# Performance work log

Hardware: AMD Instinct MI355X
Metric: run time of the kernel (lower is better)

Reference implementation:

```python
import jax, jax.numpy as jnp
import numpy as np
import math

N, L, E_IN, MDL, H, NE = 8, 4096, 512, 512, 8, 131072
D = MDL // H


def setup_inputs() -> dict:
    key = jax.random.key(0)
    ks = jax.random.split(key, 12)
    s_in = 1.0 / math.sqrt(E_IN)
    s_md = 1.0 / math.sqrt(MDL)
    return {
        "queries": jax.random.normal(ks[0], (N, L, E_IN), jnp.float32),
        "keys": jax.random.normal(ks[1], (N, L, E_IN), jnp.float32),
        "values": jax.random.normal(ks[2], (N, L, E_IN), jnp.float32),
        "adj": jax.random.randint(ks[3], (2, NE), 0, L, jnp.int32),
        "Wq": jax.random.normal(ks[4], (MDL, E_IN), jnp.float32) * s_in,
        "bq": jnp.zeros((MDL,), jnp.float32),
        "Wk": jax.random.normal(ks[5], (MDL, E_IN), jnp.float32) * s_in,
        "bk": jnp.zeros((MDL,), jnp.float32),
        "Wv": jax.random.normal(ks[6], (MDL, E_IN), jnp.float32) * s_in,
        "bv": jnp.zeros((MDL,), jnp.float32),
        "Wfc": jax.random.normal(ks[7], (MDL, MDL), jnp.float32) * s_md,
        "bfc": jnp.zeros((MDL,), jnp.float32),
    }


def _split_head(x):
    n, l, c = x.shape
    return jnp.transpose(x.reshape(n, l, H, c // H), (0, 2, 1, 3))  # (n,h,l,d)


def reference(queries, keys, values, adj, Wq, bq, Wk, bk, Wv, bv, Wfc, bfc):
    q = _split_head(queries @ Wq.T + bq)  # (n,h,l,e)
    k = _split_head(keys @ Wk.T + bk)
    v = _split_head(values @ Wv.T + bv)
    n, h, l, e = q.shape
    temp = 1.0 / math.sqrt(e)
    row, col = adj[0], adj[1]  # query idx / key idx per edge
    # edge-wise QK dot products: (n,h,E)
    qk = temp * jnp.einsum('nhed,nhed->nhe', q[:, :, row, :], k[:, :, col, :])
    # segment softmax over edges grouped by query node (adj[0])
    qk_t = jnp.transpose(qk, (2, 0, 1))  # (E,n,h) - segment ops act on axis 0
    m = jax.ops.segment_max(qk_t, row, num_segments=l)  # (L,n,h)
    ex = jnp.exp(qk_t - m[row])
    den = jax.ops.segment_sum(ex, row, num_segments=l)
    a = ex / den[row]  # (E,n,h); dropout is identity in eval mode
    # spmm: out[i] += a[edge] * v[j] for each edge (i=row, j=col)
    vj = jnp.transpose(v[:, :, col, :], (2, 0, 1, 3))  # (E,n,h,d)
    agg = jax.ops.segment_sum(vj * a[..., None], row, num_segments=l)  # (L,n,h,d)
    out = jnp.transpose(agg, (1, 0, 2, 3)).reshape(n, l, h * e)  # (n,l,h*d)
    return out @ Wfc.T + bfc
```

## Files before the change

### kernel.cpp

```cpp
#include <hip/hip_runtime.h>
#include <cstdint>

typedef __attribute__((ext_vector_type(8))) short short8;
typedef __attribute__((ext_vector_type(8))) _Float16 half8;
typedef __attribute__((ext_vector_type(2))) _Float16 h2;
typedef __attribute__((ext_vector_type(2))) __fp16 fp16x2;
typedef __attribute__((ext_vector_type(4))) float f32x4;

#define AS1 __attribute__((address_space(1)))
#define AS3 __attribute__((address_space(3)))

constexpr int NB   = 8;
constexpr int L    = 4096;
constexpr int CH   = 512;
constexpr int DD   = 64;
constexpr int NE   = 131072;
constexpr int M_ROWS = NB * L;

template <int CTRL>
__device__ __forceinline__ float dppadd(float s) {
    union { float f; int i; } u, r;
    u.f = s;
    r.i = __builtin_amdgcn_update_dpp(0, u.i, CTRL, 0xF, 0xF, true);
    return s + r.f;
}

__global__ __launch_bounds__(256)
void cvt8_k(const float* __restrict__ src, _Float16* __restrict__ dst) {
    const int i = blockIdx.x * 256 + threadIdx.x;
    const f32x4 a = ((const f32x4*)src)[i * 2];
    const f32x4 b = ((const f32x4*)src)[i * 2 + 1];
    fp16x2 h[4];
    h[0] = __builtin_amdgcn_cvt_pkrtz(a.x, a.y);
    h[1] = __builtin_amdgcn_cvt_pkrtz(a.z, a.w);
    h[2] = __builtin_amdgcn_cvt_pkrtz(b.x, b.y);
    h[3] = __builtin_amdgcn_cvt_pkrtz(b.z, b.w);
    half8 out;
    __builtin_memcpy(&out, h, 16);
    ((half8*)dst)[i] = out;
}

__global__ __launch_bounds__(256)
void cvtw_k(const float* __restrict__ s0, const float* __restrict__ s1,
            const float* __restrict__ s2, const float* __restrict__ s3,
            _Float16* __restrict__ dst) {
    const float* s = (blockIdx.y == 0) ? s0 : (blockIdx.y == 1) ? s1
                   : (blockIdx.y == 2) ? s2 : s3;
    _Float16* d = dst + (size_t)blockIdx.y * (CH * CH);
    const int i = blockIdx.x * 256 + threadIdx.x;
    const f32x4 a = ((const f32x4*)s)[i * 2];
    const f32x4 b = ((const f32x4*)s)[i * 2 + 1];
    fp16x2 h[4];
    h[0] = __builtin_amdgcn_cvt_pkrtz(a.x, a.y);
    h[1] = __builtin_amdgcn_cvt_pkrtz(a.z, a.w);
    h[2] = __builtin_amdgcn_cvt_pkrtz(b.x, b.y);
    h[3] = __builtin_amdgcn_cvt_pkrtz(b.z, b.w);
    half8 out;
    __builtin_memcpy(&out, h, 16);
    ((half8*)d)[i] = out;
}

template <bool OUT_F32>
__global__ __launch_bounds__(256)
void gemm_f16(const _Float16* __restrict__ A, const _Float16* __restrict__ B,
              const float* __restrict__ bias, void* __restrict__ Cp)
{
    __shared__ _Float16 As[128 * 64];
    __shared__ _Float16 Bs[128 * 64];
    const int bid = blockIdx.x;
    const int swz = (bid & 7) * 128 + (bid >> 3);
    const int row0 = (swz >> 2) * 128;
    const int col0 = (swz & 3) * 128;
    const int t = threadIdx.x, lane = t & 63, wid = t >> 6;
    const int wm = (wid >> 1) * 64, wn = (wid & 1) * 64;
    const int fr = lane & 15, fkb = (lane >> 4) * 8;
    const int srow = lane >> 3;
    const int scol = (lane & 7) * 8;

    f32x4 acc[4][4] = {};

    for (int k0 = 0; k0 < CH; k0 += 64) {
#pragma unroll
        for (int q = 0; q < 4; q++) {
            const int r = wid * 32 + q * 8;
            __builtin_amdgcn_global_load_lds(
                (const AS1 unsigned int*)
                    (A + (size_t)(row0 + r + srow) * CH + k0 + scol),
                (AS3 unsigned int*)(As + r * 64), 16, 0, 0);
        }
#pragma unroll
        for (int q = 0; q < 4; q++) {
            const int r = wid * 32 + q * 8;
            __builtin_amdgcn_global_load_lds(
                (const AS1 unsigned int*)
                    (B + (size_t)(col0 + r + srow) * CH + k0 + scol),
                (AS3 unsigned int*)(Bs + r * 64), 16, 0, 0);
        }
        __syncthreads();
#pragma unroll
        for (int kk = 0; kk < 2; kk++) {
            half8 afr[4], bfr[4];
#pragma unroll
            for (int f = 0; f < 4; f++)
                afr[f] = *(const half8*)&As[(wm + f * 16 + fr) * 64 + kk * 32 + fkb];
#pragma unroll
            for (int f = 0; f < 4; f++)
                bfr[f] = *(const half8*)&Bs[(wn + f * 16 + fr) * 64 + kk * 32 + fkb];
#pragma unroll
            for (int fm = 0; fm < 4; fm++)
#pragma unroll
                for (int fn = 0; fn < 4; fn++)
                    acc[fm][fn] = __builtin_amdgcn_mfma_f32_16x16x32_f16(
                        afr[fm], bfr[fn], acc[fm][fn], 0, 0, 0);
        }
        __syncthreads();
    }

    const int rsub = (lane >> 4) * 4;
#pragma unroll
    for (int fn = 0; fn < 4; fn++) {
        const int gc = col0 + wn + fn * 16 + fr;
        const float bv = bias[gc];
#pragma unroll
        for (int fm = 0; fm < 4; fm++) {
            const int gr = row0 + wm + fm * 16 + rsub;
#pragma unroll
            for (int j = 0; j < 4; j++) {
                const float v = acc[fm][fn][j] + bv;
                if constexpr (OUT_F32)
                    ((float*)Cp)[(size_t)(gr + j) * CH + gc] = v;
                else
                    ((_Float16*)Cp)[(size_t)(gr + j) * CH + gc] = (_Float16)v;
            }
        }
    }
}

__global__ void zero_k(int* cnt, int* fill) {
    int i = blockIdx.x * blockDim.x + threadIdx.x;
    if (i < L) { cnt[i] = 0; fill[i] = 0; }
}
__global__ void count_k(const int* __restrict__ adj, int* __restrict__ cnt) {
    int e = blockIdx.x * blockDim.x + threadIdx.x;
    if (e < NE) atomicAdd(&cnt[adj[e]], 1);
}
__global__ void scan_k(const int* __restrict__ cnt, int* __restrict__ rowptr) {
    const int lane = threadIdx.x;
    const int base = lane * 64;
    int s = 0;
    for (int t2 = 0; t2 < 64; t2++) s += cnt[base + t2];
    int incl = s;
    for (int off = 1; off < 64; off <<= 1) {
        int v = __shfl_up(incl, off);
        if (lane >= off) incl += v;
    }
    int run = incl - s;
    for (int t2 = 0; t2 < 64; t2++) { rowptr[base + t2] = run; run += cnt[base + t2]; }
    if (lane == 63) rowptr[L] = run;
}
__global__ void scatter_k(const int* __restrict__ adj, const int* __restrict__ rowptr,
                          int* __restrict__ fill, int* __restrict__ ecol) {
    int e = blockIdx.x * blockDim.x + threadIdx.x;
    if (e < NE) {
        int rr = adj[e];
        int pos = rowptr[rr] + atomicAdd(&fill[rr], 1);
        ecol[pos] = adj[NE + e];
    }
}

__global__ __launch_bounds__(256)
void attn_k(const _Float16* __restrict__ qb, const _Float16* __restrict__ kb,
            const _Float16* __restrict__ vb, const int* __restrict__ rowptr,
            const int* __restrict__ ecol, _Float16* __restrict__ agg)
{
    __shared__ float part[4 * 8 * 65];
    const int bid = blockIdx.x;
    const int n   = bid & 7;
    const int rem = bid >> 3;
    const int hg  = rem >> 12;
    const int i   = rem & 4095;
    const int lane = threadIdx.x & 63;
    const int w    = threadIdx.x >> 6;
    const int h    = hg * 4 + w;
    const int g    = lane & 7;
    const int grp  = lane >> 3;
    const size_t rowbase = ((size_t)(n * L + i)) * CH + h * DD;

    fp16x2 qq[4];
    {
        const half8 qu = *(const half8*)(qb + rowbase + g * 8);
        const _Float16 sc = (_Float16)(0.125f * 1.44269504088896f);
        h2 qh[4];
#pragma unroll
        for (int e = 0; e < 4; e++) {
            qh[e][0] = qu[2 * e] * sc;
            qh[e][1] = qu[2 * e + 1] * sc;
        }
        __builtin_memcpy(qq, qh, 16);
    }
    const int start = rowptr[i], end = rowptr[i + 1];
    const char* kb_u = (const char*)(kb + (size_t)n * L * CH + h * DD);
    const char* vb_u = (const char*)(vb + (size_t)n * L * CH + h * DD);
    const int goff = g << 4;

    h2 oA[4] = {}, oB[4] = {};
    float lsA = 0.f, lsB = 0.f;

    const int nIt = (end - start + 15) >> 4;
    int idx = start + grp;
    const int last = end - 1;
    half8 kA{}, vA{}, kB{}, vB{};
    int jA1 = 0, jB1 = 0;
    if (nIt > 0) {
        const int jA0 = ecol[min(idx, last)];
        const int jB0 = ecol[min(idx + 8, last)];
        kA = *(const half8*)(kb_u + ((jA0 << 10) + goff));
        vA = *(const half8*)(vb_u + ((jA0 << 10) + goff));
        kB = *(const half8*)(kb_u + ((jB0 << 10) + goff));
        vB = *(const half8*)(vb_u + ((jB0 << 10) + goff));
        jA1 = ecol[min(idx + 16, last)];
        jB1 = ecol[min(idx + 24, last)];
    }

    for (int it = 0; it < nIt; ++it) {
        const half8 kAn = *(const half8*)(kb_u + ((jA1 << 10) + goff));
        const half8 vAn = *(const half8*)(vb_u + ((jA1 << 10) + goff));
        const half8 kBn = *(const half8*)(kb_u + ((jB1 << 10) + goff));
        const half8 vBn = *(const half8*)(vb_u + ((jB1 << 10) + goff));
        const int jA2 = ecol[min(idx + 32, last)];
        const int jB2 = ecol[min(idx + 40, last)];
        const bool vdA = idx < end;
        const bool vdB = idx + 8 < end;
        fp16x2 ka[4], kb2[4];
        __builtin_memcpy(ka, &kA, 16);
        __builtin_memcpy(kb2, &kB, 16);
        float sA = 0.f, sB = 0.f;
#if __has_builtin(__builtin_amdgcn_fdot2)
#pragma unroll
        for (int e = 0; e < 4; e++) {
            sA = __builtin_amdgcn_fdot2(ka[e],  qq[e], sA, false);
            sB = __builtin_amdgcn_fdot2(kb2[e], qq[e], sB, false);
        }
#else
#pragma unroll
        for (int e = 0; e < 4; e++) {
            sA = fmaf((float)ka[e][0],  (float)qq[e][0], sA);
            sA = fmaf((float)ka[e][1],  (float)qq[e][1], sA);
            sB = fmaf((float)kb2[e][0], (float)qq[e][0], sB);
            sB = fmaf((float)kb2[e][1], (float)qq[e][1], sB);
        }
#endif
        sA = dppadd<0xB1>(sA);  sB = dppadd<0xB1>(sB);
        sA = dppadd<0x4E>(sA);  sB = dppadd<0x4E>(sB);
        sA = dppadd<0x141>(sA); sB = dppadd<0x141>(sB);
        float peA = exp2f(sA); peA = vdA ? peA : 0.f;
        float peB = exp2f(sB); peB = vdB ? peB : 0.f;
        const _Float16 phA = (_Float16)peA, phB = (_Float16)peB;
        const h2 pa2 = {phA, phA}, pb2 = {phB, phB};
        h2 va2[4], vb2[4];
        __builtin_memcpy(va2, &vA, 16);
        __builtin_memcpy(vb2, &vB, 16);
#pragma unroll
        for (int e = 0; e < 4; e++) {
            oA[e] += pa2 * va2[e];
            oB[e] += pb2 * vb2[e];
        }
        lsA += peA; lsB += peB;
        kA = kAn; vA = vAn; kB = kBn; vB = vBn;
        jA1 = jA2; jB1 = jB2; idx += 16;
    }

    float lsum = lsA + lsB;
    lsum += __shfl_xor(lsum, 8);
    lsum += __shfl_xor(lsum, 16);
    lsum += __shfl_xor(lsum, 32);

    float o[8];
#pragma unroll
    for (int e = 0; e < 4; e++) {
        o[2 * e]     = (float)oA[e][0] + (float)oB[e][0];
        o[2 * e + 1] = (float)oA[e][1] + (float)oB[e][1];
    }
    float* p = part + w * (8 * 65);
    float* pw = p + grp * 65 + g * 8;
    *(f32x4*)(pw)     = *(f32x4*)&o[0];
    *(f32x4*)(pw + 4) = *(f32x4*)&o[4];
    __builtin_amdgcn_s_waitcnt(0);
    float osum = 0.f;
#pragma unroll
    for (int gg = 0; gg < 8; gg++)
        osum += p[gg * 65 + lane];

    const float inv = (end > start) ? 1.f / lsum : 0.f;
    agg[rowbase + lane] = (_Float16)(osum * inv);
}

extern "C" void kernel_launch(void* const* d_in, const int* in_sizes, int n_in,
                              void* d_out, int out_size, void* d_ws, size_t ws_size,
                              hipStream_t stream)
{
    (void)in_sizes; (void)n_in; (void)out_size; (void)ws_size;
    const float* queries = (const float*)d_in[0];
    const float* keys    = (const float*)d_in[1];
    const float* values  = (const float*)d_in[2];
    const int*   adj     = (const int*)d_in[3];
    const float* Wq  = (const float*)d_in[4];
    const float* bq  = (const float*)d_in[5];
    const float* Wk  = (const float*)d_in[6];
    const float* bk  = (const float*)d_in[7];
    const float* Wv  = (const float*)d_in[8];
    const float* bv  = (const float*)d_in[9];
    const float* Wfc = (const float*)d_in[10];
    const float* bfc = (const float*)d_in[11];

    _Float16* qb = (_Float16*)d_out;
    _Float16* kb = qb + (size_t)M_ROWS * CH;
    uint8_t* w = (uint8_t*)d_ws;
    _Float16* vb  = (_Float16*)(w);
    _Float16* agg = (_Float16*)(w + 33554432);
    _Float16* wf  = (_Float16*)(w + 67108864);
    int* cnt    = (int*)(w + 69206016);
    int* fill   = (int*)(w + 69206016 + 16384);
    int* rowptr = (int*)(w + 69206016 + 32768);
    int* ecol   = (int*)(w + 69206016 + 65536);

    _Float16* stg = agg;
    constexpr int WELEM = CH * CH;

    cvtw_k<<<dim3(WELEM / (256 * 8), 4), 256, 0, stream>>>(Wq, Wk, Wv, Wfc, wf);

    zero_k<<<(L + 255) / 256, 256, 0, stream>>>(cnt, fill);
    count_k<<<(NE + 255) / 256, 256, 0, stream>>>(adj, cnt);
    scan_k<<<1, 64, 0, stream>>>(cnt, rowptr);
    scatter_k<<<(NE + 255) / 256, 256, 0, stream>>>(adj, rowptr, fill, ecol);

    dim3 gg(1024);
    cvt8_k<<<M_ROWS * CH / (256 * 8), 256, 0, stream>>>(queries, stg);
    gemm_f16<false><<<gg, 256, 0, stream>>>(stg, wf + 0 * WELEM, bq, qb);
    cvt8_k<<<M_ROWS * CH / (256 * 8), 256, 0, stream>>>(keys, stg);
    gemm_f16<false><<<gg, 256, 0, stream>>>(stg, wf + 1 * WELEM, bk, kb);
    cvt8_k<<<M_ROWS * CH / (256 * 8), 256, 0, stream>>>(values, stg);
    gemm_f16<false><<<gg, 256, 0, stream>>>(stg, wf + 2 * WELEM, bv, vb);

    attn_k<<<dim3(2 * NB * L), 256, 0, stream>>>(qb, kb, vb, rowptr, ecol, agg);

    gemm_f16<true><<<gg, 256, 0, stream>>>(agg, wf + 3 * WELEM, bfc, (float*)d_out);
}
```

Before: 344.8 us.

## Fuse independent prep stages into horizontally merged kernels with double staging

Merges the weight conversion, CSR construction steps and input conversions into four horizontally fused launches. Each GEMM for Q/K/V shares its grid with the fp16 conversion of the next input, using a second staging buffer. This cuts the number of launches and lets memory-bound conversion blocks overlap with MFMA GEMM blocks. The fused path only runs if the workspace is large enough; otherwise the old sequence is kept. Fused kernels reserve GEMM shared memory even for conversion blocks, which may limit their occupancy.

```diff
diff --git a/kernel.cpp b/kernel.cpp
--- a/kernel.cpp
+++ b/kernel.cpp
@@ -16,6 +16,7 @@
 constexpr int DD   = 64;
 constexpr int NE   = 131072;
 constexpr int M_ROWS = NB * L;
+constexpr int WELEM  = CH * CH;
 
 template <int CTRL>
 __device__ __forceinline__ float dppadd(float s) {
@@ -25,9 +26,10 @@
     return s + r.f;
 }
 
-__global__ __launch_bounds__(256)
-void cvt8_k(const float* __restrict__ src, _Float16* __restrict__ dst) {
-    const int i = blockIdx.x * 256 + threadIdx.x;
+
+__device__ __forceinline__ void cvt_body(int bid, const float* __restrict__ src,
+                                         _Float16* __restrict__ dst) {
+    const int i = bid * 256 + (int)threadIdx.x;
     const f32x4 a = ((const f32x4*)src)[i * 2];
     const f32x4 b = ((const f32x4*)src)[i * 2 + 1];
     fp16x2 h[4];
@@ -40,14 +42,88 @@
     ((half8*)dst)[i] = out;
 }
 
-__global__ __launch_bounds__(256)
-void cvtw_k(const float* __restrict__ s0, const float* __restrict__ s1,
-            const float* __restrict__ s2, const float* __restrict__ s3,
-            _Float16* __restrict__ dst) {
-    const float* s = (blockIdx.y == 0) ? s0 : (blockIdx.y == 1) ? s1
-                   : (blockIdx.y == 2) ? s2 : s3;
-    _Float16* d = dst + (size_t)blockIdx.y * (CH * CH);
-    const int i = blockIdx.x * 256 + threadIdx.x;
+template <bool OUT_F32>
+__device__ __forceinline__ void gemm_body(int bid, _Float16* As, _Float16* Bs,
+                                          const _Float16* __restrict__ A,
+                                          const _Float16* __restrict__ B,
+                                          const float* __restrict__ bias,
+                                          void* __restrict__ Cp)
+{
+    const int swz = (bid & 7) * 128 + (bid >> 3);
+    const int row0 = (swz >> 2) * 128;
+    const int col0 = (swz & 3) * 128;
+    const int t = threadIdx.x, lane = t & 63, wid = t >> 6;
+    const int wm = (wid >> 1) * 64, wn = (wid & 1) * 64;
+    const int fr = lane & 15, fkb = (lane >> 4) * 8;
+    const int srow = lane >> 3;
+    const int scol = (lane & 7) * 8;
+
+    f32x4 acc[4][4] = {};
+
+    for (int k0 = 0; k0 < CH; k0 += 64) {
+#pragma unroll
+        for (int q = 0; q < 4; q++) {
+            const int r = wid * 32 + q * 8;
+            __builtin_amdgcn_global_load_lds(
+                (const AS1 unsigned int*)
+                    (A + (size_t)(row0 + r + srow) * CH + k0 + scol),
+                (AS3 unsigned int*)(As + r * 64), 16, 0, 0);
+        }
+#pragma unroll
+        for (int q = 0; q < 4; q++) {
+            const int r = wid * 32 + q * 8;
+            __builtin_amdgcn_global_load_lds(
+                (const AS1 unsigned int*)
+                    (B + (size_t)(col0 + r + srow) * CH + k0 + scol),
+                (AS3 unsigned int*)(Bs + r * 64), 16, 0, 0);
+        }
+        __syncthreads();
+#pragma unroll
+        for (int kk = 0; kk < 2; kk++) {
+            half8 afr[4], bfr[4];
+#pragma unroll
+            for (int f = 0; f < 4; f++)
+                afr[f] = *(const half8*)&As[(wm + f * 16 + fr) * 64 + kk * 32 + fkb];
+#pragma unroll
+            for (int f = 0; f < 4; f++)
+                bfr[f] = *(const half8*)&Bs[(wn + f * 16 + fr) * 64 + kk * 32 + fkb];
+#pragma unroll
+            for (int fm = 0; fm < 4; fm++)
+#pragma unroll
+                for (int fn = 0; fn < 4; fn++)
+                    acc[fm][fn] = __builtin_amdgcn_mfma_f32_16x16x32_f16(
+                        afr[fm], bfr[fn], acc[fm][fn], 0, 0, 0);
+        }
+        __syncthreads();
+    }
+
+    const int rsub = (lane >> 4) * 4;
+#pragma unroll
+    for (int fn = 0; fn < 4; fn++) {
+        const int gc = col0 + wn + fn * 16 + fr;
+        const float bv = bias[gc];
+#pragma unroll
+        for (int fm = 0; fm < 4; fm++) {
+            const int gr = row0 + wm + fm * 16 + rsub;
+#pragma unroll
+            for (int j = 0; j < 4; j++) {
+                const float v = acc[fm][fn][j] + bv;
+                if constexpr (OUT_F32)
+                    ((float*)Cp)[(size_t)(gr + j) * CH + gc] = v;
+                else
+                    ((_Float16*)Cp)[(size_t)(gr + j) * CH + gc] = (_Float16)v;
+            }
+        }
+    }
+}
+
+__device__ __forceinline__ void cvtw_body(int bid, const float* s0, const float* s1,
+                                          const float* s2, const float* s3,
+                                          _Float16* dst) {
+    const int idx = bid * 256 + (int)threadIdx.x;
+    const int wsel = idx >> 15;
+    const float* s = (wsel == 0) ? s0 : (wsel == 1) ? s1 : (wsel == 2) ? s2 : s3;
+    const int i = idx & 32767;
     const f32x4 a = ((const f32x4*)s)[i * 2];
     const f32x4 b = ((const f32x4*)s)[i * 2 + 1];
     fp16x2 h[4];
@@ -57,95 +133,20 @@
     h[3] = __builtin_amdgcn_cvt_pkrtz(b.z, b.w);
     half8 out;
     __builtin_memcpy(&out, h, 16);
-    ((half8*)d)[i] = out;
-}
-
-template <bool OUT_F32>
-__global__ __launch_bounds__(256)
-void gemm_f16(const _Float16* __restrict__ A, const _Float16* __restrict__ B,
-              const float* __restrict__ bias, void* __restrict__ Cp)
-{
-    __shared__ _Float16 As[128 * 64];
-    __shared__ _Float16 Bs[128 * 64];
-    const int bid = blockIdx.x;
-    const int swz = (bid & 7) * 128 + (bid >> 3);
-    const int row0 = (swz >> 2) * 128;
-    const int col0 = (swz & 3) * 128;
-    const int t = threadIdx.x, lane = t & 63, wid = t >> 6;
-    const int wm = (wid >> 1) * 64, wn = (wid & 1) * 64;
-    const int fr = lane & 15, fkb = (lane >> 4) * 8;
-    const int srow = lane >> 3;
-    const int scol = (lane & 7) * 8;
-
-    f32x4 acc[4][4] = {};
-
-    for (int k0 = 0; k0 < CH; k0 += 64) {
-#pragma unroll
-        for (int q = 0; q < 4; q++) {
-            const int r = wid * 32 + q * 8;
-            __builtin_amdgcn_global_load_lds(
-                (const AS1 unsigned int*)
-                    (A + (size_t)(row0 + r + srow) * CH + k0 + scol),
-                (AS3 unsigned int*)(As + r * 64), 16, 0, 0);
-        }
-#pragma unroll
-        for (int q = 0; q < 4; q++) {
-            const int r = wid * 32 + q * 8;
-            __builtin_amdgcn_global_load_lds(
-                (const AS1 unsigned int*)
-                    (B + (size_t)(col0 + r + srow) * CH + k0 + scol),
-                (AS3 unsigned int*)(Bs + r * 64), 16, 0, 0);
-        }
-        __syncthreads();
-#pragma unroll
-        for (int kk = 0; kk < 2; kk++) {
-            half8 afr[4], bfr[4];
-#pragma unroll
-            for (int f = 0; f < 4; f++)
-                afr[f] = *(const half8*)&As[(wm + f * 16 + fr) * 64 + kk * 32 + fkb];
-#pragma unroll
-            for (int f = 0; f < 4; f++)
-                bfr[f] = *(const half8*)&Bs[(wn + f * 16 + fr) * 64 + kk * 32 + fkb];
-#pragma unroll
-            for (int fm = 0; fm < 4; fm++)
-#pragma unroll
-                for (int fn = 0; fn < 4; fn++)
-                    acc[fm][fn] = __builtin_amdgcn_mfma_f32_16x16x32_f16(
-                        afr[fm], bfr[fn], acc[fm][fn], 0, 0, 0);
-        }
-        __syncthreads();
-    }
-
-    const int rsub = (lane >> 4) * 4;
-#pragma unroll
-    for (int fn = 0; fn < 4; fn++) {
-        const int gc = col0 + wn + fn * 16 + fr;
-        const float bv = bias[gc];
-#pragma unroll
-        for (int fm = 0; fm < 4; fm++) {
-            const int gr = row0 + wm + fm * 16 + rsub;
-#pragma unroll
-            for (int j = 0; j < 4; j++) {
-                const float v = acc[fm][fn][j] + bv;
-                if constexpr (OUT_F32)
-                    ((float*)Cp)[(size_t)(gr + j) * CH + gc] = v;
-                else
-                    ((_Float16*)Cp)[(size_t)(gr + j) * CH + gc] = (_Float16)v;
-            }
-        }
-    }
-}
-
-__global__ void zero_k(int* cnt, int* fill) {
-    int i = blockIdx.x * blockDim.x + threadIdx.x;
+    ((half8*)(dst + (size_t)wsel * WELEM))[i] = out;
+}
+
+__device__ __forceinline__ void zero_body(int bid, int* cnt, int* fill) {
+    const int i = bid * 256 + (int)threadIdx.x;
     if (i < L) { cnt[i] = 0; fill[i] = 0; }
 }
-__global__ void count_k(const int* __restrict__ adj, int* __restrict__ cnt) {
-    int e = blockIdx.x * blockDim.x + threadIdx.x;
+__device__ __forceinline__ void count_body(int bid, const int* adj, int* cnt) {
+    const int e = bid * 256 + (int)threadIdx.x;
     if (e < NE) atomicAdd(&cnt[adj[e]], 1);
 }
-__global__ void scan_k(const int* __restrict__ cnt, int* __restrict__ rowptr) {
+__device__ __forceinline__ void scan_body(const int* cnt, int* rowptr) {
     const int lane = threadIdx.x;
+    if (lane >= 64) return;
     const int base = lane * 64;
     int s = 0;
     for (int t2 = 0; t2 < 64; t2++) s += cnt[base + t2];
@@ -158,14 +159,95 @@
     for (int t2 = 0; t2 < 64; t2++) { rowptr[base + t2] = run; run += cnt[base + t2]; }
     if (lane == 63) rowptr[L] = run;
 }
-__global__ void scatter_k(const int* __restrict__ adj, const int* __restrict__ rowptr,
-                          int* __restrict__ fill, int* __restrict__ ecol) {
-    int e = blockIdx.x * blockDim.x + threadIdx.x;
+__device__ __forceinline__ void scatter_body(int bid, const int* adj, const int* rowptr,
+                                             int* fill, int* ecol) {
+    const int e = bid * 256 + (int)threadIdx.x;
     if (e < NE) {
         int rr = adj[e];
         int pos = rowptr[rr] + atomicAdd(&fill[rr], 1);
         ecol[pos] = adj[NE + e];
     }
+}
+
+__global__ __launch_bounds__(256)
+void fusedD0(const float* __restrict__ queries, _Float16* __restrict__ stgA,
+             const float* Wq, const float* Wk, const float* Wv, const float* Wfc,
+             _Float16* __restrict__ wf, int* cnt, int* fill)
+{
+    const int bid = blockIdx.x;
+    if (bid < 8192)       cvt_body(bid, queries, stgA);
+    else if (bid < 8704)  cvtw_body(bid - 8192, Wq, Wk, Wv, Wfc, wf);
+    else                  zero_body(bid - 8704, cnt, fill);
+}
+
+__global__ __launch_bounds__(256)
+void fusedD1(const _Float16* __restrict__ stgA, const _Float16* __restrict__ wf,
+             const float* __restrict__ bq, _Float16* __restrict__ qb,
+             const float* __restrict__ keys, _Float16* __restrict__ stgB,
+             const int* __restrict__ adj, int* cnt)
+{
+    __shared__ _Float16 As[128 * 64];
+    __shared__ _Float16 Bs[128 * 64];
+    const int bid = blockIdx.x;
+    if (bid < 1024)       gemm_body<false>(bid, As, Bs, stgA, wf, bq, qb);
+    else if (bid < 9216)  cvt_body(bid - 1024, keys, stgB);
+    else                  count_body(bid - 9216, adj, cnt);
+}
+
+__global__ __launch_bounds__(256)
+void fusedD2(const _Float16* __restrict__ stgB, const _Float16* __restrict__ wf,
+             const float* __restrict__ bk, _Float16* __restrict__ kb,
+             const float* __restrict__ values, _Float16* __restrict__ stgA,
+             const int* __restrict__ cnt, int* rowptr)
+{
+    __shared__ _Float16 As[128 * 64];
+    __shared__ _Float16 Bs[128 * 64];
+    const int bid = blockIdx.x;
+    if (bid < 1024)       gemm_body<false>(bid, As, Bs, stgB, wf, bk, kb);
+    else if (bid < 9216)  cvt_body(bid - 1024, values, stgA);
+    else                  scan_body(cnt, rowptr);
+}
+
+__global__ __launch_bounds__(256)
+void fusedD3(const _Float16* __restrict__ stgA, const _Float16* __restrict__ wf,
+             const float* __restrict__ bv, _Float16* __restrict__ vb,
+             const int* __restrict__ adj, const int* __restrict__ rowptr,
+             int* fill, int* ecol)
+{
+    __shared__ _Float16 As[128 * 64];
+    __shared__ _Float16 Bs[128 * 64];
+    const int bid = blockIdx.x;
+    if (bid < 1024)  gemm_body<false>(bid, As, Bs, stgA, wf, bv, vb);
+    else             scatter_body(bid - 1024, adj, rowptr, fill, ecol);
+}
+
+__global__ __launch_bounds__(256)
+void cvt8_k(const float* __restrict__ src, _Float16* __restrict__ dst) {
+    cvt_body(blockIdx.x, src, dst);
+}
+__global__ __launch_bounds__(256)
+void cvtw_k(const float* Wq, const float* Wk, const float* Wv, const float* Wfc,
+            _Float16* wf) {
+    cvtw_body(blockIdx.x, Wq, Wk, Wv, Wfc, wf);
+}
+__global__ __launch_bounds__(256)
+void zero_k(int* cnt, int* fill) { zero_body(blockIdx.x, cnt, fill); }
+__global__ __launch_bounds__(256)
+void count_k(const int* adj, int* cnt) { count_body(blockIdx.x, adj, cnt); }
+__global__ __launch_bounds__(256)
+void scan_k(const int* cnt, int* rowptr) { scan_body(cnt, rowptr); }
+__global__ __launch_bounds__(256)
+void scatter_k(const int* adj, const int* rowptr, int* fill, int* ecol) {
+    scatter_body(blockIdx.x, adj, rowptr, fill, ecol);
+}
+template <bool OUT_F32>
+__global__ __launch_bounds__(256)
+void gemm_f16(const _Float16* __restrict__ A, const _Float16* __restrict__ B,
+              const float* __restrict__ bias, void* __restrict__ Cp)
+{
+    __shared__ _Float16 As[128 * 64];
+    __shared__ _Float16 Bs[128 * 64];
+    gemm_body<OUT_F32>(blockIdx.x, As, Bs, A, B, bias, Cp);
 }
 
 __global__ __launch_bounds__(256)
@@ -299,7 +381,7 @@
                               void* d_out, int out_size, void* d_ws, size_t ws_size,
                               hipStream_t stream)
 {
-    (void)in_sizes; (void)n_in; (void)out_size; (void)ws_size;
+    (void)in_sizes; (void)n_in; (void)out_size;
     const float* queries = (const float*)d_in[0];
     const float* keys    = (const float*)d_in[1];
     const float* values  = (const float*)d_in[2];
@@ -316,33 +398,44 @@
     _Float16* qb = (_Float16*)d_out;
     _Float16* kb = qb + (size_t)M_ROWS * CH;
     uint8_t* w = (uint8_t*)d_ws;
-    _Float16* vb  = (_Float16*)(w);
-    _Float16* agg = (_Float16*)(w + 33554432);
-    _Float16* wf  = (_Float16*)(w + 67108864);
+    _Float16* vb   = (_Float16*)(w);
+    _Float16* stgA = (_Float16*)(w + 33554432);
+    _Float16* agg  = stgA;
+    _Float16* wf   = (_Float16*)(w + 67108864);
     int* cnt    = (int*)(w + 69206016);
     int* fill   = (int*)(w + 69206016 + 16384);
     int* rowptr = (int*)(w + 69206016 + 32768);
     int* ecol   = (int*)(w + 69206016 + 65536);
-
-    _Float16* stg = agg;
-    constexpr int WELEM = CH * CH;
-
-    cvtw_k<<<dim3(WELEM / (256 * 8), 4), 256, 0, stream>>>(Wq, Wk, Wv, Wfc, wf);
-
-    zero_k<<<(L + 255) / 256, 256, 0, stream>>>(cnt, fill);
-    count_k<<<(NE + 255) / 256, 256, 0, stream>>>(adj, cnt);
-    scan_k<<<1, 64, 0, stream>>>(cnt, rowptr);
-    scatter_k<<<(NE + 255) / 256, 256, 0, stream>>>(adj, rowptr, fill, ecol);
-
-    dim3 gg(1024);
-    cvt8_k<<<M_ROWS * CH / (256 * 8), 256, 0, stream>>>(queries, stg);
-    gemm_f16<false><<<gg, 256, 0, stream>>>(stg, wf + 0 * WELEM, bq, qb);
-    cvt8_k<<<M_ROWS * CH / (256 * 8), 256, 0, stream>>>(keys, stg);
-    gemm_f16<false><<<gg, 256, 0, stream>>>(stg, wf + 1 * WELEM, bk, kb);
-    cvt8_k<<<M_ROWS * CH / (256 * 8), 256, 0, stream>>>(values, stg);
-    gemm_f16<false><<<gg, 256, 0, stream>>>(stg, wf + 2 * WELEM, bv, vb);
-
-    attn_k<<<dim3(2 * NB * L), 256, 0, stream>>>(qb, kb, vb, rowptr, ecol, agg);
-
-    gemm_f16<true><<<gg, 256, 0, stream>>>(agg, wf + 3 * WELEM, bfc, (float*)d_out);
-}
+    _Float16* stgB = (_Float16*)(w + 69795840);
+    constexpr size_t WS_NEED = 69795840ull + 33554432ull;
+
+    if (ws_size >= WS_NEED) {
+        fusedD0<<<dim3(8720), 256, 0, stream>>>(queries, stgA, Wq, Wk, Wv, Wfc,
+                                                wf, cnt, fill);
+        fusedD1<<<dim3(9728), 256, 0, stream>>>(stgA, wf + 0 * WELEM, bq, qb,
+                                                keys, stgB, adj, cnt);
+        fusedD2<<<dim3(9217), 256, 0, stream>>>(stgB, wf + 1 * WELEM, bk, kb,
+                                                values, stgA, cnt, rowptr);
+        fusedD3<<<dim3(1536), 256, 0, stream>>>(stgA, wf + 2 * WELEM, bv, vb,
+                                                adj, rowptr, fill, ecol);
+        attn_k<<<dim3(2 * NB * L), 256, 0, stream>>>(qb, kb, vb, rowptr, ecol, agg);
+        gemm_f16<true><<<dim3(1024), 256, 0, stream>>>(agg, wf + 3 * WELEM, bfc,
+                                                       (float*)d_out);
+    } else {
+        _Float16* stg = stgA;
+        cvtw_k<<<dim3(512), 256, 0, stream>>>(Wq, Wk, Wv, Wfc, wf);
+        zero_k<<<dim3(16), 256, 0, stream>>>(cnt, fill);
+        count_k<<<dim3(512), 256, 0, stream>>>(adj, cnt);
+        scan_k<<<dim3(1), 256, 0, stream>>>(cnt, rowptr);
+        scatter_k<<<dim3(512), 256, 0, stream>>>(adj, rowptr, fill, ecol);
+        cvt8_k<<<dim3(8192), 256, 0, stream>>>(queries, stg);
+        gemm_f16<false><<<dim3(1024), 256, 0, stream>>>(stg, wf + 0 * WELEM, bq, qb);
+        cvt8_k<<<dim3(8192), 256, 0, stream>>>(keys, stg);
+        gemm_f16<false><<<dim3(1024), 256, 0, stream>>>(stg, wf + 1 * WELEM, bk, kb);
+        cvt8_k<<<dim3(8192), 256, 0, stream>>>(values, stg);
+        gemm_f16<false><<<dim3(1024), 256, 0, stream>>>(stg, wf + 2 * WELEM, bv, vb);
+        attn_k<<<dim3(2 * NB * L), 256, 0, stream>>>(qb, kb, vb, rowptr, ecol, agg);
+        gemm_f16<true><<<dim3(1024), 256, 0, stream>>>(agg, wf + 3 * WELEM, bfc,
+                                                       (float*)d_out);
+    }
+}
```

After: 308.7 us (median of 2 runs). -10.5%, faster.
